# Kernel tuning notes

Hardware: AMD Instinct MI355X
Metric: run time of the kernel (lower is better)

The kernel has to match this reference:

```python
import jax, jax.numpy as jnp
import numpy as np

E, N, C = 8192, 512, 1024
SILU_CST = 1.6790524  # e3nn normalize2mom constant for SiLU (2nd-moment normalization)


def setup_inputs() -> dict:
    key = jax.random.key(0)
    ks = jax.random.split(key, 9)
    return {
        "edge_features": jax.random.normal(ks[0], (E, C), jnp.float32),
        "node_features": jax.random.normal(ks[1], (N, C), jnp.float32),
        "edge_index": jax.random.randint(ks[2], (2, E), 0, N),
        # GATConv params (heads=1): lin weight (no bias), att vectors, output bias
        "gat_lin_w": jax.random.normal(ks[3], (C, C), jnp.float32) / np.float32(np.sqrt(C)),
        "att_src": jax.random.normal(ks[4], (C,), jnp.float32) / np.float32(np.sqrt(C)),
        "att_dst": jax.random.normal(ks[5], (C,), jnp.float32) / np.float32(np.sqrt(C)),
        "gat_bias": jnp.zeros((C,), jnp.float32),
        # ScalarMLPFunction weights, 'uniform' init in [-sqrt(3), sqrt(3)]
        "mlp_w0": jax.random.uniform(ks[6], (C, C), jnp.float32, -np.sqrt(3), np.sqrt(3)),
        "mlp_w1": jax.random.uniform(ks[7], (C, C), jnp.float32, -np.sqrt(3), np.sqrt(3)),
    }


def _gat(x, edge_index, W, a_s, a_d, b):
    # Artificial graph: node u_e per original edge e; directed artificial edge j->i
    # iff src[j]==src[i], j<i, and neither j nor i is a self-loop edge. PyG GATConv
    # then adds self-loops for ALL E artificial nodes.
    src, dst = edge_index[0], edge_index[1]
    valid = src != dst  # self-loop removal mask on original edges
    h = x @ W                      # [E, C] shared src/dst transform (heads=1)
    al_s = h @ a_s                 # [E] alpha_src
    al_d = h @ a_d                 # [E] alpha_dst
    idx = jnp.arange(x.shape[0])
    same_src = (src[:, None] == src[None, :]) & valid[:, None] & valid[None, :]
    art = same_src & (idx[:, None] < idx[None, :])          # strict upper triangle
    mask = art | (idx[:, None] == idx[None, :])             # + GATConv self-loops
    # logits[j, i]: message from artificial node j to target i
    logits = jnp.where(mask, jax.nn.leaky_relu(al_s[:, None] + al_d[None, :], 0.2), -jnp.inf)
    alpha = jax.nn.softmax(logits, axis=0)  # softmax over sources j, per target i
    return jnp.einsum('ji,jc->ic', alpha, h) + b  # [E, C]


def _mlp(x, w0, w1):
    # ScalarMLPFunction: w scaled by norm_from_last / sqrt(h_in); silu between layers
    h = jax.nn.silu(x @ (w0 * (1.0 / np.float32(np.sqrt(C)))))
    return h @ (w1 * np.float32(SILU_CST / np.sqrt(C)))


def reference(edge_features, node_features, edge_index, gat_lin_w, att_src, att_dst,
              gat_bias, mlp_w0, mlp_w1):
    new_edge_features = _gat(edge_features, edge_index, gat_lin_w, att_src, att_dst, gat_bias)
    new_node_features = _mlp(node_features, mlp_w0, mlp_w1)
    return new_edge_features, new_node_features
```

## Files before the change

### kernel.cpp

```cpp
#include <hip/hip_runtime.h>
#include <hip/hip_bf16.h>
#include <stdint.h>

#define C_DIM 1024
#define MAXG 96

typedef __attribute__((ext_vector_type(8))) __bf16 bf16x8;
typedef __attribute__((ext_vector_type(8))) short short8;
typedef __attribute__((ext_vector_type(4))) float f32x4;

__device__ __forceinline__ short f2bf(float f) {
  unsigned u = __float_as_uint(f);
  unsigned r = (u + 0x7fffu + ((u >> 16) & 1u)) >> 16;
  return (short)r;
}
__device__ __forceinline__ float bf2f(short s) {
  return __uint_as_float(((unsigned)(unsigned short)s) << 16);
}

__device__ __forceinline__ void gload_lds16(const void* g, void* lds) {
  __builtin_amdgcn_global_load_lds(
      (const __attribute__((address_space(1))) unsigned int*)g,
      (__attribute__((address_space(3))) unsigned int*)lds,
      16, 0, 0);
}

__global__ void cvt_bf16(const float* __restrict__ in, short* __restrict__ out, int n4) {
  int i = blockIdx.x * blockDim.x + threadIdx.x;
  if (i < n4) {
    float4 v = ((const float4*)in)[i];
    short4 o;
    o.x = f2bf(v.x); o.y = f2bf(v.y); o.z = f2bf(v.z); o.w = f2bf(v.w);
    ((short4*)out)[i] = o;
  }
}

__global__ void transpose_cvt(const float* __restrict__ in, short* __restrict__ out, float scale) {
  __shared__ float tile[32][33];
  int bx = blockIdx.x * 32, by = blockIdx.y * 32;
  int x = threadIdx.x, y4 = threadIdx.y * 4;
#pragma unroll
  for (int r = 0; r < 4; ++r)
    tile[y4 + r][x] = in[(size_t)(by + y4 + r) * C_DIM + bx + x];
  __syncthreads();
#pragma unroll
  for (int r = 0; r < 4; ++r)
    out[(size_t)(bx + y4 + r) * C_DIM + by + x] = f2bf(tile[x][y4 + r] * scale);
}

template <int EPI, int BM, int BN>
__global__ __launch_bounds__(256)
void gemm_bt(const short* __restrict__ A, const short* __restrict__ Bt,
             float* __restrict__ Cf, short* __restrict__ Cb,
             int M, int N, int K) {
  constexpr int WR = BM / 2, WC = BN / 2;
  constexpr int MT = WR / 16, NT = WC / 16;
  __shared__ __align__(16) short sA[BM * 32];
  __shared__ __align__(16) short sB[BN * 32];
  const int t = threadIdx.x;
  const int wave = t >> 6, lane = t & 63;
  const int wm = wave >> 1, wn = wave & 1;
  const int bm = blockIdx.x, bn = blockIdx.y;
  const int rm = lane & 15, kg = lane >> 4;

  f32x4 acc[MT][NT];
#pragma unroll
  for (int i = 0; i < MT; ++i)
#pragma unroll
    for (int j = 0; j < NT; ++j) acc[i][j] = f32x4{0.f, 0.f, 0.f, 0.f};

  const size_t Abase = (size_t)bm * BM * K;
  const size_t Bbase = (size_t)bn * BN * K;
  const int nk = K >> 5;

  for (int kk = 0; kk < nk; ++kk) {
    const int k0 = kk << 5;
#pragma unroll
    for (int i = 0; i < BM / 64; ++i) {
      int c = i * 256 + t;
      gload_lds16(A + Abase + (size_t)(c >> 2) * K + k0 + (c & 3) * 8,
                  &sA[(i * 256 + wave * 64) * 8]);
    }
#pragma unroll
    for (int i = 0; i < BN / 64; ++i) {
      int c = i * 256 + t;
      gload_lds16(Bt + Bbase + (size_t)(c >> 2) * K + k0 + (c & 3) * 8,
                  &sB[(i * 256 + wave * 64) * 8]);
    }
    __syncthreads();

    short8 af[MT], bfv[NT];
#pragma unroll
    for (int mt = 0; mt < MT; ++mt)
      af[mt] = *(const short8*)&sA[(wm * WR + mt * 16 + rm) * 32 + kg * 8];
#pragma unroll
    for (int nt = 0; nt < NT; ++nt)
      bfv[nt] = *(const short8*)&sB[(wn * WC + nt * 16 + rm) * 32 + kg * 8];
#pragma unroll
    for (int mt = 0; mt < MT; ++mt)
#pragma unroll
      for (int nt = 0; nt < NT; ++nt)
        acc[mt][nt] = __builtin_amdgcn_mfma_f32_16x16x32_bf16(
            __builtin_bit_cast(bf16x8, af[mt]),
            __builtin_bit_cast(bf16x8, bfv[nt]), acc[mt][nt], 0, 0, 0);
    __syncthreads();
  }

  const int row0 = bm * BM + wm * WR;
  const int col0 = bn * BN + wn * WC;
#pragma unroll
  for (int mt = 0; mt < MT; ++mt)
#pragma unroll
    for (int nt = 0; nt < NT; ++nt) {
      f32x4 v = acc[mt][nt];
      int r0 = row0 + mt * 16 + kg * 4;
      int cc = col0 + nt * 16 + rm;
#pragma unroll
      for (int j = 0; j < 4; ++j) {
        float x = v[j];
        if (EPI == 1) {
          float s = x / (1.f + __expf(-x));
          Cb[(size_t)(r0 + j) * N + cc] = f2bf(s);
        } else if (EPI == 2) {
          Cb[(size_t)(r0 + j) * N + cc] = f2bf(x);
        } else {
          Cf[(size_t)(r0 + j) * N + cc] = x;
        }
      }
    }
}

__global__ __launch_bounds__(256)
void al_kernel(const short* __restrict__ H, const float* __restrict__ as,
               const float* __restrict__ ad, float* __restrict__ als,
               float* __restrict__ ald) {
  int row = blockIdx.x * 4 + (threadIdx.x >> 6);
  int lane = threadIdx.x & 63;
  float ss = 0.f, sd = 0.f;
  for (int q = lane * 8; q < C_DIM; q += 512) {
    short8 hv = *(const short8*)&H[(size_t)row * C_DIM + q];
#pragma unroll
    for (int j = 0; j < 8; ++j) {
      float hf = bf2f(hv[j]);
      ss += hf * as[q + j];
      sd += hf * ad[q + j];
    }
  }
#pragma unroll
  for (int off = 32; off > 0; off >>= 1) {
    ss += __shfl_down(ss, off);
    sd += __shfl_down(sd, off);
  }
  if (lane == 0) { als[row] = ss; ald[row] = sd; }
}

__global__ __launch_bounds__(256)
void group_build(const int* __restrict__ src, const int* __restrict__ dst,
                 int* __restrict__ glist, int* __restrict__ epos, int E) {
  const int s = blockIdx.x;
  const int t = threadIdx.x;
  const int lane = t & 63, w = t >> 6;
  __shared__ int cnt;
  __shared__ int wsum[4];
  if (t == 0) cnt = 0;
  __syncthreads();
  for (int base = 0; base < E; base += 256) {
    int e = base + t;
    bool m = (src[e] == s) && (dst[e] != s);
    unsigned long long bmask = __ballot(m);
    if (lane == 0) wsum[w] = __popcll(bmask);
    __syncthreads();
    int off = cnt;
    for (int ww = 0; ww < w; ++ww) off += wsum[ww];
    int p = off + __popcll(bmask & ((1ull << lane) - 1ull));
    if (m) {
      if (p < MAXG) { glist[s * MAXG + p] = e; epos[e] = p; }
      else epos[e] = MAXG;
    }
    __syncthreads();
    if (t == 0) cnt = min(MAXG, cnt + wsum[0] + wsum[1] + wsum[2] + wsum[3]);
    __syncthreads();
  }
}

__global__ __launch_bounds__(256)
void attn_out(const int* __restrict__ src, const int* __restrict__ dst,
              const short* __restrict__ H, const float* __restrict__ als,
              const float* __restrict__ ald, const int* __restrict__ glist,
              const int* __restrict__ epos, const float* __restrict__ bias,
              float* __restrict__ out) {
  const int i = blockIdx.x;
  const int t = threadIdx.x;
  const int s = src[i];
  const int c0 = t * 4;
  if (s == dst[i]) {
    short4 hv = *(const short4*)&H[(size_t)i * C_DIM + c0];
    float4 b4 = *(const float4*)&bias[c0];
    float4 o;
    o.x = bf2f(hv.x) + b4.x; o.y = bf2f(hv.y) + b4.y;
    o.z = bf2f(hv.z) + b4.z; o.w = bf2f(hv.w) + b4.w;
    *(float4*)&out[(size_t)i * C_DIM + c0] = o;
    return;
  }
  __shared__ int eid[MAXG + 1];
  __shared__ float ash[MAXG + 1];
  __shared__ float alv[MAXG + 1];
  const int p = epos[i];
  if (t < p) {
    int e = glist[s * MAXG + t];
    eid[t] = e;
    ash[t] = als[e];
  }
  if (t == 0) { eid[p] = i; ash[p] = als[i]; }
  __syncthreads();
  const int L = p + 1;
  const float adi = ald[i];
  float mx = -1e30f;
  for (int q = 0; q < L; ++q) {
    float x = ash[q] + adi;
    x = x > 0.f ? x : 0.2f * x;
    mx = fmaxf(mx, x);
  }
  float ssum = 0.f;
  for (int q = 0; q < L; ++q) {
    float x = ash[q] + adi;
    x = x > 0.f ? x : 0.2f * x;
    ssum += __expf(x - mx);
  }
  float rs = 1.f / ssum;
  if (t < L) {
    float x = ash[t] + adi;
    x = x > 0.f ? x : 0.2f * x;
    alv[t] = __expf(x - mx) * rs;
  }
  __syncthreads();
  float4 acc = *(const float4*)&bias[c0];
  for (int q = 0; q < L; ++q) {
    float a = alv[q];
    short4 hv = *(const short4*)&H[(size_t)eid[q] * C_DIM + c0];
    acc.x += a * bf2f(hv.x); acc.y += a * bf2f(hv.y);
    acc.z += a * bf2f(hv.z); acc.w += a * bf2f(hv.w);
  }
  *(float4*)&out[(size_t)i * C_DIM + c0] = acc;
}

extern "C" void kernel_launch(void* const* d_in, const int* in_sizes, int n_in,
                              void* d_out, int out_size, void* d_ws, size_t ws_size,
                              hipStream_t stream) {
  const float* edge_f = (const float*)d_in[0];
  const float* node_f = (const float*)d_in[1];
  const int*   eidx   = (const int*)d_in[2];
  const float* gat_w  = (const float*)d_in[3];
  const float* att_s  = (const float*)d_in[4];
  const float* att_d  = (const float*)d_in[5];
  const float* gat_b  = (const float*)d_in[6];
  const float* w0     = (const float*)d_in[7];
  const float* w1     = (const float*)d_in[8];

  const int E = in_sizes[0] / C_DIM;
  const int N = in_sizes[1] / C_DIM;
  const int NSRC = 512;
  const int* src = eidx;
  const int* dst = eidx + E;
  float* out_edge = (float*)d_out;
  float* out_node = out_edge + (size_t)E * C_DIM;

  char* ws = (char*)d_ws;
  short* Xb  = (short*)ws; ws += (size_t)E * C_DIM * 2;
  short* Wt  = (short*)ws; ws += (size_t)C_DIM * C_DIM * 2;
  short* W0t = (short*)ws; ws += (size_t)C_DIM * C_DIM * 2;
  short* W1t = (short*)ws; ws += (size_t)C_DIM * C_DIM * 2;
  short* Xnb = (short*)ws; ws += (size_t)N * C_DIM * 2;
  short* H1b = (short*)ws; ws += (size_t)N * C_DIM * 2;
  short* H   = (short*)ws; ws += (size_t)E * C_DIM * 2;
  float* ALs = (float*)ws; ws += (size_t)E * 4;
  float* ALd = (float*)ws; ws += (size_t)E * 4;
  int*   Glist = (int*)ws; ws += (size_t)NSRC * MAXG * 4;
  int*   Epos  = (int*)ws; ws += (size_t)E * 4;

  group_build<<<dim3(NSRC), 256, 0, stream>>>(src, dst, Glist, Epos, E);

  dim3 tb(32, 8);
  cvt_bf16<<<dim3((E * C_DIM / 4 + 255) / 256), 256, 0, stream>>>(edge_f, Xb, E * C_DIM / 4);
  cvt_bf16<<<dim3((N * C_DIM / 4 + 255) / 256), 256, 0, stream>>>(node_f, Xnb, N * C_DIM / 4);
  transpose_cvt<<<dim3(32, 32), tb, 0, stream>>>(gat_w, Wt, 1.0f);
  transpose_cvt<<<dim3(32, 32), tb, 0, stream>>>(w0, W0t, 0.03125f);
  transpose_cvt<<<dim3(32, 32), tb, 0, stream>>>(w1, W1t, 1.6790524f * 0.03125f);

  gemm_bt<2, 128, 128><<<dim3(E / 128, C_DIM / 128), 256, 0, stream>>>(
      Xb, Wt, nullptr, H, E, C_DIM, C_DIM);
  al_kernel<<<dim3(E / 4), 256, 0, stream>>>(H, att_s, att_d, ALs, ALd);
  attn_out<<<dim3(E), 256, 0, stream>>>(src, dst, H, ALs, ALd, Glist, Epos, gat_b, out_edge);

  gemm_bt<1, 64, 64><<<dim3(N / 64, C_DIM / 64), 256, 0, stream>>>(
      Xnb, W0t, nullptr, H1b, N, C_DIM, C_DIM);
  gemm_bt<0, 64, 64><<<dim3(N / 64, C_DIM / 64), 256, 0, stream>>>(
      H1b, W1t, out_node, nullptr, N, C_DIM, C_DIM);
}
```

Baseline: 218.6 us.

## Parallelize group build, merge weight transposes, deepen GEMM K-tile, remap workgroups

Replaces the per-source group_build kernel, which had 512 blocks each scanning all edges, with a chunked histogram plus scatter pass that computes the same per-source ordering positions. Merges the three weight transpose launches into one 3D-grid launch. The GEMM now stages 64-wide K tiles instead of 32, halving the barrier count per K, and remaps the flat block index so that consecutive blocks are spread across the eight XCDs. These changes aim to cut launch count, the redundant scanning cost and GEMM synchronization, at the price of more LDS per block and a serial prefix loop inside the scatter kernel.

```diff
diff --git a/kernel.cpp b/kernel.cpp
--- a/kernel.cpp
+++ b/kernel.cpp
@@ -4,6 +4,8 @@
 
 #define C_DIM 1024
 #define MAXG 96
+#define NSRC 512
+#define NCHUNK 32
 
 typedef __attribute__((ext_vector_type(8))) __bf16 bf16x8;
 typedef __attribute__((ext_vector_type(8))) short short8;
@@ -35,8 +37,15 @@
   }
 }
 
-__global__ void transpose_cvt(const float* __restrict__ in, short* __restrict__ out, float scale) {
+__global__ void transpose_cvt3(const float* __restrict__ in0, const float* __restrict__ in1,
+                               const float* __restrict__ in2, short* __restrict__ out0,
+                               short* __restrict__ out1, short* __restrict__ out2,
+                               float s0, float s1, float s2) {
   __shared__ float tile[32][33];
+  const int z = blockIdx.z;
+  const float* in = z == 0 ? in0 : (z == 1 ? in1 : in2);
+  short* out = z == 0 ? out0 : (z == 1 ? out1 : out2);
+  const float scale = z == 0 ? s0 : (z == 1 ? s1 : s2);
   int bx = blockIdx.x * 32, by = blockIdx.y * 32;
   int x = threadIdx.x, y4 = threadIdx.y * 4;
 #pragma unroll
@@ -52,15 +61,17 @@
 __global__ __launch_bounds__(256)
 void gemm_bt(const short* __restrict__ A, const short* __restrict__ Bt,
              float* __restrict__ Cf, short* __restrict__ Cb,
-             int M, int N, int K) {
+             int M, int N, int K, int gm ) {
   constexpr int WR = BM / 2, WC = BN / 2;
   constexpr int MT = WR / 16, NT = WC / 16;
-  __shared__ __align__(16) short sA[BM * 32];
-  __shared__ __align__(16) short sB[BN * 32];
+  __shared__ __align__(16) short sA[BM * 64];
+  __shared__ __align__(16) short sB[BN * 64];
   const int t = threadIdx.x;
   const int wave = t >> 6, lane = t & 63;
   const int wm = wave >> 1, wn = wave & 1;
-  const int bm = blockIdx.x, bn = blockIdx.y;
+  const int nwg = gridDim.x, q = nwg >> 3;
+  const int wg = (blockIdx.x & 7) * q + (blockIdx.x >> 3);
+  const int bm = wg % gm, bn = wg / gm;
   const int rm = lane & 15, kg = lane >> 4;
 
   f32x4 acc[MT][NT];
@@ -71,38 +82,41 @@
 
   const size_t Abase = (size_t)bm * BM * K;
   const size_t Bbase = (size_t)bn * BN * K;
-  const int nk = K >> 5;
+  const int nk = K >> 6;
 
   for (int kk = 0; kk < nk; ++kk) {
-    const int k0 = kk << 5;
-#pragma unroll
-    for (int i = 0; i < BM / 64; ++i) {
+    const int k0 = kk << 6;
+#pragma unroll
+    for (int i = 0; i < BM / 32; ++i) {
       int c = i * 256 + t;
-      gload_lds16(A + Abase + (size_t)(c >> 2) * K + k0 + (c & 3) * 8,
+      gload_lds16(A + Abase + (size_t)(c >> 3) * K + k0 + (c & 7) * 8,
                   &sA[(i * 256 + wave * 64) * 8]);
     }
 #pragma unroll
-    for (int i = 0; i < BN / 64; ++i) {
+    for (int i = 0; i < BN / 32; ++i) {
       int c = i * 256 + t;
-      gload_lds16(Bt + Bbase + (size_t)(c >> 2) * K + k0 + (c & 3) * 8,
+      gload_lds16(Bt + Bbase + (size_t)(c >> 3) * K + k0 + (c & 7) * 8,
                   &sB[(i * 256 + wave * 64) * 8]);
     }
     __syncthreads();
 
-    short8 af[MT], bfv[NT];
-#pragma unroll
-    for (int mt = 0; mt < MT; ++mt)
-      af[mt] = *(const short8*)&sA[(wm * WR + mt * 16 + rm) * 32 + kg * 8];
-#pragma unroll
-    for (int nt = 0; nt < NT; ++nt)
-      bfv[nt] = *(const short8*)&sB[(wn * WC + nt * 16 + rm) * 32 + kg * 8];
-#pragma unroll
-    for (int mt = 0; mt < MT; ++mt)
+#pragma unroll
+    for (int kk2 = 0; kk2 < 2; ++kk2) {
+      short8 af[MT], bfv[NT];
+#pragma unroll
+      for (int mt = 0; mt < MT; ++mt)
+        af[mt] = *(const short8*)&sA[(wm * WR + mt * 16 + rm) * 64 + kk2 * 32 + kg * 8];
 #pragma unroll
       for (int nt = 0; nt < NT; ++nt)
-        acc[mt][nt] = __builtin_amdgcn_mfma_f32_16x16x32_bf16(
-            __builtin_bit_cast(bf16x8, af[mt]),
-            __builtin_bit_cast(bf16x8, bfv[nt]), acc[mt][nt], 0, 0, 0);
+        bfv[nt] = *(const short8*)&sB[(wn * WC + nt * 16 + rm) * 64 + kk2 * 32 + kg * 8];
+#pragma unroll
+      for (int mt = 0; mt < MT; ++mt)
+#pragma unroll
+        for (int nt = 0; nt < NT; ++nt)
+          acc[mt][nt] = __builtin_amdgcn_mfma_f32_16x16x32_bf16(
+              __builtin_bit_cast(bf16x8, af[mt]),
+              __builtin_bit_cast(bf16x8, bfv[nt]), acc[mt][nt], 0, 0, 0);
+    }
     __syncthreads();
   }
 
@@ -155,32 +169,40 @@
 }
 
 __global__ __launch_bounds__(256)
-void group_build(const int* __restrict__ src, const int* __restrict__ dst,
-                 int* __restrict__ glist, int* __restrict__ epos, int E) {
-  const int s = blockIdx.x;
-  const int t = threadIdx.x;
-  const int lane = t & 63, w = t >> 6;
-  __shared__ int cnt;
-  __shared__ int wsum[4];
-  if (t == 0) cnt = 0;
-  __syncthreads();
-  for (int base = 0; base < E; base += 256) {
-    int e = base + t;
-    bool m = (src[e] == s) && (dst[e] != s);
-    unsigned long long bmask = __ballot(m);
-    if (lane == 0) wsum[w] = __popcll(bmask);
-    __syncthreads();
-    int off = cnt;
-    for (int ww = 0; ww < w; ++ww) off += wsum[ww];
-    int p = off + __popcll(bmask & ((1ull << lane) - 1ull));
-    if (m) {
-      if (p < MAXG) { glist[s * MAXG + p] = e; epos[e] = p; }
-      else epos[e] = MAXG;
-    }
-    __syncthreads();
-    if (t == 0) cnt = min(MAXG, cnt + wsum[0] + wsum[1] + wsum[2] + wsum[3]);
-    __syncthreads();
-  }
+void group_hist(const int* __restrict__ src, const int* __restrict__ dst,
+                int* __restrict__ hist) {
+  __shared__ int h[NSRC];
+  const int b = blockIdx.x, t = threadIdx.x;
+  h[t] = 0; h[t + 256] = 0;
+  __syncthreads();
+  int e = b * 256 + t;
+  int s = src[e];
+  bool m = (s != dst[e]);
+  if (m) atomicAdd(&h[s], 1);
+  __syncthreads();
+  hist[(size_t)t * NCHUNK + b] = h[t];
+  hist[(size_t)(t + 256) * NCHUNK + b] = h[t + 256];
+}
+
+__global__ __launch_bounds__(256)
+void group_scatter(const int* __restrict__ src, const int* __restrict__ dst,
+                   const int* __restrict__ hist, int* __restrict__ glist,
+                   int* __restrict__ epos) {
+  __shared__ int ssrc[256];
+  __shared__ unsigned char sval[256];
+  const int b = blockIdx.x, t = threadIdx.x;
+  int e = b * 256 + t;
+  int s = src[e];
+  bool m = (s != dst[e]);
+  ssrc[t] = s;
+  sval[t] = m ? 1 : 0;
+  __syncthreads();
+  if (!m) return;
+  int p = 0;
+  for (int c = 0; c < b; ++c) p += hist[(size_t)s * NCHUNK + c];
+  for (int j = 0; j < t; ++j) p += (ssrc[j] == s) & sval[j];
+  if (p < MAXG) { glist[s * MAXG + p] = e; epos[e] = p; }
+  else epos[e] = MAXG;
 }
 
 __global__ __launch_bounds__(256)
@@ -259,7 +281,6 @@
 
   const int E = in_sizes[0] / C_DIM;
   const int N = in_sizes[1] / C_DIM;
-  const int NSRC = 512;
   const int* src = eidx;
   const int* dst = eidx + E;
   float* out_edge = (float*)d_out;
@@ -277,23 +298,23 @@
   float* ALd = (float*)ws; ws += (size_t)E * 4;
   int*   Glist = (int*)ws; ws += (size_t)NSRC * MAXG * 4;
   int*   Epos  = (int*)ws; ws += (size_t)E * 4;
-
-  group_build<<<dim3(NSRC), 256, 0, stream>>>(src, dst, Glist, Epos, E);
-
-  dim3 tb(32, 8);
+  int*   Hist  = (int*)ws; ws += (size_t)NSRC * NCHUNK * 4;
+
+  group_hist<<<dim3(NCHUNK), 256, 0, stream>>>(src, dst, Hist);
+  group_scatter<<<dim3(NCHUNK), 256, 0, stream>>>(src, dst, Hist, Glist, Epos);
+
   cvt_bf16<<<dim3((E * C_DIM / 4 + 255) / 256), 256, 0, stream>>>(edge_f, Xb, E * C_DIM / 4);
   cvt_bf16<<<dim3((N * C_DIM / 4 + 255) / 256), 256, 0, stream>>>(node_f, Xnb, N * C_DIM / 4);
-  transpose_cvt<<<dim3(32, 32), tb, 0, stream>>>(gat_w, Wt, 1.0f);
-  transpose_cvt<<<dim3(32, 32), tb, 0, stream>>>(w0, W0t, 0.03125f);
-  transpose_cvt<<<dim3(32, 32), tb, 0, stream>>>(w1, W1t, 1.6790524f * 0.03125f);
-
-  gemm_bt<2, 128, 128><<<dim3(E / 128, C_DIM / 128), 256, 0, stream>>>(
-      Xb, Wt, nullptr, H, E, C_DIM, C_DIM);
+  transpose_cvt3<<<dim3(32, 32, 3), dim3(32, 8), 0, stream>>>(
+      gat_w, w0, w1, Wt, W0t, W1t, 1.0f, 0.03125f, 1.6790524f * 0.03125f);
+
+  gemm_bt<2, 128, 128><<<dim3((E / 128) * (C_DIM / 128)), 256, 0, stream>>>(
+      Xb, Wt, nullptr, H, E, C_DIM, C_DIM, E / 128);
   al_kernel<<<dim3(E / 4), 256, 0, stream>>>(H, att_s, att_d, ALs, ALd);
   attn_out<<<dim3(E), 256, 0, stream>>>(src, dst, H, ALs, ALd, Glist, Epos, gat_b, out_edge);
 
-  gemm_bt<1, 64, 64><<<dim3(N / 64, C_DIM / 64), 256, 0, stream>>>(
-      Xnb, W0t, nullptr, H1b, N, C_DIM, C_DIM);
-  gemm_bt<0, 64, 64><<<dim3(N / 64, C_DIM / 64), 256, 0, stream>>>(
-      H1b, W1t, out_node, nullptr, N, C_DIM, C_DIM);
-}
+  gemm_bt<1, 64, 64><<<dim3((N / 64) * (C_DIM / 64)), 256, 0, stream>>>(
+      Xnb, W0t, nullptr, H1b, N, C_DIM, C_DIM, N / 64);
+  gemm_bt<0, 64, 64><<<dim3((N / 64) * (C_DIM / 64)), 256, 0, stream>>>(
+      H1b, W1t, out_node, nullptr, N, C_DIM, C_DIM, N / 64);
+}
```

After: 205.3 us. -6.1%, faster.
